# Performance work log

Measured on AMD Instinct MI355X. Metric: run time of the kernel, lower is better.

## Reference

```python
import jax, jax.numpy as jnp
import numpy as np

B, C, H, W = 16, 2, 768, 768
WIN = 5                      # window_size: maxima kernel AND gauss-fit window
PAD = WIN // 2
HEATMAP_AXIS = 1
THRESHOLD = 0.5
MAX_DET = 393216             # fixed-size pad for data-dependent nonzero()


def setup_inputs() -> dict:
    key = jax.random.key(0)
    # strictly positive heat so log(z) in Guo's fit is well-defined
    x = jax.random.uniform(key, (B, C, H, W), dtype=jnp.float32, minval=1e-4, maxval=1.0)
    return {"x": x}


def _forward(x):
    heat = x[:, HEATMAP_AXIS]                                   # [B,H,W]
    th = jnp.where(heat > THRESHOLD, heat, 0.0)
    # kornia dilation with ones kernel (center zeroed) == max over neighbors excl. center
    padded = jnp.pad(th, ((0, 0), (PAD, PAD), (PAD, PAD)), constant_values=-np.inf)
    dilated = jnp.full(th.shape, -np.inf, th.dtype)
    for dy in range(WIN):
        for dx in range(WIN):
            if dy == PAD and dx == PAD:
                continue
            dilated = jnp.maximum(dilated, padded[:, dy:dy + H, dx:dx + W])
    local_max = (th > dilated).reshape(-1)                      # strict local maxima above threshold
    (flat_idx,) = jnp.nonzero(local_max, size=MAX_DET, fill_value=0)  # row-major, like torch.nonzero
    valid = jnp.arange(MAX_DET) < local_max.sum()
    bidx = flat_idx // (H * W)
    rc = flat_idx % (H * W)
    r = rc // W
    cc = rc % W
    sub = jnp.linspace((-WIN) // 2 + 1, WIN // 2, WIN)
    xs, ys = jnp.meshgrid(sub, sub, indexing='xy')              # xs varies along columns
    xf = xs.reshape(-1).astype(jnp.float32)                     # [K]
    yf = ys.reshape(-1).astype(jnp.float32)
    off = jnp.arange(WIN) - PAD
    off_r = jnp.repeat(off, WIN)                                # row-major window flattening
    off_c = jnp.tile(off, WIN)
    rows = jnp.clip(r[:, None] + off_r[None, :], 0, H - 1)      # clamp at borders
    cols = jnp.clip(cc[:, None] + off_c[None, :], 0, W - 1)
    z = heat[bidx[:, None], rows, cols]                         # [N,K] window intensities
    z = jnp.clip(z, 1e-6, None)                                 # numerical guard for log
    xb = jnp.broadcast_to(xf, z.shape)
    yb = jnp.broadcast_to(yf, z.shape)
    # quadratic basis [1, x, x^2, y, xy, y^2]
    basis = jnp.stack([jnp.ones_like(xb), xb, xb * xb, yb, xb * yb, yb * yb], -1)  # [N,K,6]
    wgt = z * z                                                  # Guo's weights
    Aw = basis * wgt[:, :, None]
    bvec = jnp.log(z) * wgt
    ATA = jnp.einsum('nki,nkj->nij', Aw, Aw)                     # [N,6,6]
    ATb = jnp.einsum('nki,nk->ni', Aw, bvec)                     # [N,6]
    coef = jnp.einsum('nij,nj->ni', jnp.linalg.inv(ATA), ATb)    # [N,6]
    Aq, Bl, Cc = coef[:, [2, 5]], coef[:, [1, 3]], coef[:, [0, 4]]
    good = valid & jnp.all(Aq < 0, axis=-1)                      # concave fit -> real sigma
    g = good[:, None]
    Aq_s = jnp.where(g, Aq, -0.5)                                # guard against NaN at padded slots
    sigma = jnp.sqrt(-1.0 / (2.0 * Aq_s))
    mu = Bl * sigma ** 2
    height = jnp.exp(jnp.where(g, Cc + 0.5 * mu ** 2 / sigma ** 2, 0.0))
    pos = jnp.stack([r, cc], -1).astype(jnp.float32) + mu[:, ::-1]  # maxima_indices + mu[:,[1,0]]
    sigma = jnp.where(g, sigma, 0.0)
    pos = jnp.where(g, pos, 0.0)
    height = jnp.where(g, height, 0.0)
    return sigma, pos, height, good


def reference(x):
    return _forward(x)
```

## Files before the change

### kernel.cpp

```cpp
#include <hip/hip_runtime.h>
#include <hip/hip_bf16.h>
#include <cstdint>

#define BATCH 16
#define HDIM 768
#define WDIM 768
#define HW (HDIM * WDIM)
#define NPIX (BATCH * HW)
#define MAX_DET 393216
#define NWORDS (NPIX / 64)
#define SCAT_BLOCKS 576
#define WPB 256

#define MASK_OFF 0u
#define CNT_OFF  1179648u
#define OFF_OFF  1183744u
#define TOT_OFF  1187840u
#define IDX_OFF  1188096u

#define SIGMA_BASE 0
#define POS_BASE   786432
#define HGT_BASE   1572864
#define GOOD_BASE  2359296

#define TILE_C 256
#define TILE_R 32
#define LDS_C 264
#define LDS_R 36
#define VEC_PER_ROW 66
#define TOT_VEC (LDS_R * VEC_PER_ROW)

__device__ __forceinline__ double fast_log_f32(float zf) {
    int ib = __float_as_int(zf);
    int e = ((ib >> 23) & 255) - 127;
    float m1 = __int_as_float((ib & 0x007fffff) | 0x3f800000);
    if (m1 > 1.41421356237f) { m1 *= 0.5f; e += 1; }
    double md = (double)m1;
    double num = md - 1.0;
    double den = md + 1.0;
    double r = (double)__builtin_amdgcn_rcpf((float)den);
    r = r * (2.0 - den * r);
    double s = num * r;
    double t = s * s;
    double P = 1.1111111111111110e-01;
    P = fma(P, t, 1.4285714285714285e-01);
    P = fma(P, t, 2.0000000000000001e-01);
    P = fma(P, t, 3.3333333333333331e-01);
    double s2 = s + s;
    double lm = fma(s2, t * P, s2);
    return fma((double)e, 0.6931471805599453, lm);
}

__device__ __forceinline__ double fast_rcp(double d) {
    double r = (double)__builtin_amdgcn_rcpf((float)d);
    r = r * (2.0 - d * r);
    r = r * (2.0 - d * r);
    return r;
}

__global__ __launch_bounds__(256) void mask_kernel(const float* __restrict__ x,
                                                   unsigned long long* __restrict__ mask) {
    __shared__ float lds[LDS_R * LDS_C];
    const int bid = blockIdx.x;
    const int b   = bid / 72;
    const int rem = bid - b * 72;
    const int rt  = rem / 3;
    const int cs  = rem - rt * 3;
    const int r0  = rt * TILE_R;
    const int tid = threadIdx.x;
    const float* heat = x + (size_t)b * (2 * HW) + HW;

    const int colbase = cs * TILE_C - 4;
    #pragma unroll
    for (int i = 0; i < 10; ++i) {
        int idx = i * 256 + tid;
        if (idx < TOT_VEC) {
            int lr = (unsigned)idx / VEC_PER_ROW;
            int q  = idx - lr * VEC_PER_ROW;
            int row = r0 - 2 + lr;
            int col = colbase + 4 * q;
            float4 v = make_float4(0.f, 0.f, 0.f, 0.f);
            if (row >= 0 && row < HDIM && col >= 0 && col <= WDIM - 4) {
                v = *reinterpret_cast<const float4*>(heat + (size_t)row * WDIM + col);
            }
            float4 t;
            t.x = v.x > 0.5f ? v.x : 0.f;
            t.y = v.y > 0.5f ? v.y : 0.f;
            t.z = v.z > 0.5f ? v.z : 0.f;
            t.w = v.w > 0.5f ? v.w : 0.f;
            *reinterpret_cast<float4*>(&lds[lr * LDS_C + 4 * q]) = t;
        }
    }
    __syncthreads();

    const int wv   = tid >> 6;
    const int lane = tid & 63;
    const int lrow0 = wv * 8;

    auto readrow = [&](int ldsrow, float* h5, float* hx, float* tc) {
        const float* p = &lds[ldsrow * LDS_C + 4 * lane];
        float4 a = *reinterpret_cast<const float4*>(p);
        float4 bb = *reinterpret_cast<const float4*>(p + 4);
        float4 cc = *reinterpret_cast<const float4*>(p + 8);
        float t2=a.z,t3=a.w,t4=bb.x,t5=bb.y,t6=bb.z,t7=bb.w,t8=cc.x,t9=cc.y;
        float pp0=fmaxf(t2,t3), pp1=fmaxf(t3,t4), pp2=fmaxf(t4,t5), pp3=fmaxf(t5,t6),
              pp4=fmaxf(t6,t7), pp5=fmaxf(t7,t8), pp6=fmaxf(t8,t9);
        h5[0]=fmaxf(fmaxf(pp0,pp2),t6);  hx[0]=fmaxf(pp0,pp3);  tc[0]=t4;
        h5[1]=fmaxf(fmaxf(pp1,pp3),t7);  hx[1]=fmaxf(pp1,pp4);  tc[1]=t5;
        h5[2]=fmaxf(fmaxf(pp2,pp4),t8);  hx[2]=fmaxf(pp2,pp5);  tc[2]=t6;
        h5[3]=fmaxf(fmaxf(pp3,pp5),t9);  hx[3]=fmaxf(pp3,pp6);  tc[3]=t7;
    };

    float h5r[5][4], hxr[5][4], tcr[5][4];
    #pragma unroll
    for (int j = 0; j < 4; ++j)
        readrow(lrow0 + j, h5r[j], hxr[j], tcr[j]);

    const int wordbase = b * (HW / 64) + (r0 + wv * 8) * 12 + cs * 4;

    #pragma unroll
    for (int k = 0; k < 8; ++k) {
        readrow(lrow0 + k + 4, h5r[(k+4)%5], hxr[(k+4)%5], tcr[(k+4)%5]);
        unsigned nib = 0;
        #pragma unroll
        for (int c = 0; c < 4; ++c) {
            float dil = fmaxf(fmaxf(h5r[k%5][c], h5r[(k+1)%5][c]),
                        fmaxf(hxr[(k+2)%5][c],
                        fmaxf(h5r[(k+3)%5][c], h5r[(k+4)%5][c])));
            if (tcr[(k+2)%5][c] > dil) nib |= (1u << c);
        }
        unsigned long long w = (unsigned long long)nib << ((lane & 15) * 4);
        w |= __shfl_xor(w, 1);
        w |= __shfl_xor(w, 2);
        w |= __shfl_xor(w, 4);
        w |= __shfl_xor(w, 8);
        if ((lane & 15) == 0) mask[wordbase + k * 12 + (lane >> 4)] = w;
    }
}

__global__ __launch_bounds__(WPB) void count_kernel(const unsigned long long* __restrict__ mask,
                                                    int* __restrict__ counts) {
    __shared__ int s[WPB];
    int t = threadIdx.x;
    int w = blockIdx.x * WPB + t;
    s[t] = __popcll(mask[w]);
    __syncthreads();
    for (int off = WPB / 2; off > 0; off >>= 1) {
        if (t < off) s[t] += s[t + off];
        __syncthreads();
    }
    if (t == 0) counts[blockIdx.x] = s[0];
}

__global__ __launch_bounds__(SCAT_BLOCKS) void scan_kernel(const int* __restrict__ counts,
                                                           int* __restrict__ offsets,
                                                           int* __restrict__ total) {
    __shared__ int s[SCAT_BLOCKS];
    int t = threadIdx.x;
    int my = counts[t];
    s[t] = my;
    __syncthreads();
    for (int off = 1; off < SCAT_BLOCKS; off <<= 1) {
        int add = (t >= off) ? s[t - off] : 0;
        __syncthreads();
        s[t] += add;
        __syncthreads();
    }
    offsets[t] = s[t] - my;
    if (t == SCAT_BLOCKS - 1) *total = s[t];
}

__global__ __launch_bounds__(WPB) void scatter_kernel(const unsigned long long* __restrict__ mask,
                                                      const int* __restrict__ offsets,
                                                      int* __restrict__ flat_idx) {
    __shared__ int s[WPB];
    int t = threadIdx.x;
    int w = blockIdx.x * WPB + t;
    unsigned long long m = mask[w];
    int cnt = __popcll(m);
    s[t] = cnt;
    __syncthreads();
    for (int off = 1; off < WPB; off <<= 1) {
        int add = (t >= off) ? s[t - off] : 0;
        __syncthreads();
        s[t] += add;
        __syncthreads();
    }
    int base = offsets[blockIdx.x] + s[t] - cnt;
    int idx0 = w << 6;
    while (m) {
        int j = __builtin_ctzll(m);
        if (base < MAX_DET) flat_idx[base] = idx0 + j;
        ++base;
        m &= m - 1;
    }
}

__global__ __launch_bounds__(256) void fit_kernel(const float* __restrict__ x,
                                                  const int* __restrict__ flat_idx,
                                                  const int* __restrict__ total,
                                                  float* __restrict__ out) {
    int n = blockIdx.x * 256 + threadIdx.x;
    int count = *total;
    float sx = 0.f, sy = 0.f, p0 = 0.f, p1 = 0.f, h0 = 0.f, h1 = 0.f, goodf = 0.f;
    if (n < count) {
        int idx = flat_idx[n];
        int b = idx / HW;
        int rc = idx - b * HW;
        int r = rc / WDIM;
        int c = rc - r * WDIM;
        const float* heat = x + (size_t)b * (2 * HW) + HW;

        double M00=0,M10=0,M01=0,M20=0,M11=0,M02=0,M30=0,M21=0,M12=0,M03=0;
        double M40=0,M31=0,M22=0,M13=0,M04=0;
        double N0=0,N1=0,N2=0,N3=0,N4=0,N5=0;
        #pragma unroll
        for (int dy = -2; dy <= 2; ++dy) {
            int rr = min(max(r + dy, 0), HDIM - 1);
            const float* hp = heat + (size_t)rr * WDIM;
            double S0=0,S1=0,S2=0,S3=0,S4=0,T0=0,T1=0,T2=0;
            #pragma unroll
            for (int dx = -2; dx <= 2; ++dx) {
                int cc = min(max(c + dx, 0), WDIM - 1);
                float zf = fmaxf(hp[cc], 1e-6f);
                double z = (double)zf;
                double z2 = z * z;
                double w2 = z2 * z2;
                double wl = w2 * fast_log_f32(zf);
                const double X = (double)dx;
                S0 += w2; T0 += wl;
                if (dx != 0) {
                    S1 += w2 * X;
                    S2 += w2 * (X * X);
                    S3 += w2 * (X * X * X);
                    S4 += w2 * (X * X * X * X);
                    T1 += wl * X;
                    T2 += wl * (X * X);
                }
            }
            const double Y = (double)dy;
            M00 += S0; M10 += S1; M20 += S2; M30 += S3; M40 += S4;
            N0 += T0; N1 += T1; N2 += T2;
            if (dy != 0) {
                double Y2 = Y * Y, Y3 = Y2 * Y, Y4 = Y2 * Y2;
                M01 += S0 * Y;  M11 += S1 * Y;  M21 += S2 * Y;  M31 += S3 * Y;
                M02 += S0 * Y2; M12 += S1 * Y2; M22 += S2 * Y2;
                M03 += S0 * Y3; M13 += S1 * Y3;
                M04 += S0 * Y4;
                N3 += T0 * Y; N4 += T1 * Y; N5 += T0 * Y2;
            }
        }

        double A[6][7];
        A[0][0]=M00; A[0][1]=M10; A[0][2]=M20; A[0][3]=M01; A[0][4]=M11; A[0][5]=M02; A[0][6]=N0;
        A[1][0]=M10; A[1][1]=M20; A[1][2]=M30; A[1][3]=M11; A[1][4]=M21; A[1][5]=M12; A[1][6]=N1;
        A[2][0]=M20; A[2][1]=M30; A[2][2]=M40; A[2][3]=M21; A[2][4]=M31; A[2][5]=M22; A[2][6]=N2;
        A[3][0]=M01; A[3][1]=M11; A[3][2]=M21; A[3][3]=M02; A[3][4]=M12; A[3][5]=M03; A[3][6]=N3;
        A[4][0]=M11; A[4][1]=M21; A[4][2]=M31; A[4][3]=M12; A[4][4]=M22; A[4][5]=M13; A[4][6]=N4;
        A[5][0]=M02; A[5][1]=M12; A[5][2]=M22; A[5][3]=M03; A[5][4]=M13; A[5][5]=M04; A[5][6]=N5;

        #pragma unroll
        for (int i = 0; i < 6; ++i) {
            double inv = fast_rcp(A[i][i]);
            #pragma unroll
            for (int j = i + 1; j < 7; ++j) A[i][j] *= inv;
            #pragma unroll
            for (int ii = i + 1; ii < 6; ++ii) {
                double f = A[ii][i];
                #pragma unroll
                for (int j = i + 1; j < 7; ++j) A[ii][j] -= f * A[i][j];
            }
        }
        double cv[6];
        #pragma unroll
        for (int i = 5; i >= 0; --i) {
            double v = A[i][6];
            #pragma unroll
            for (int j = i + 1; j < 6; ++j) v -= A[i][j] * cv[j];
            cv[i] = v;
        }

        double aqx = cv[2], aqy = cv[5];
        if (aqx < 0.0 && aqy < 0.0) {
            double sx2 = -0.5 * fast_rcp(aqx);
            double sy2 = -0.5 * fast_rcp(aqy);
            sx2 = fmin(sx2, 1e300);
            sy2 = fmin(sy2, 1e300);
            double sigx = sqrt(sx2), sigy = sqrt(sy2);
            double mux = cv[1] * sx2, muy = cv[3] * sy2;
            sx = (float)sigx;
            sy = (float)sigy;
            p0 = (float)((double)r + muy);
            p1 = (float)((double)c + mux);
            double hv0 = exp(cv[0] + 0.5 * cv[1] * cv[1] * sx2);
            double hv1 = exp(cv[4] + 0.5 * cv[3] * cv[3] * sy2);
            if (!(hv0 <= 3.0e38)) hv0 = 3.0e38;
            if (!(hv1 <= 3.0e38)) hv1 = 3.0e38;
            h0 = (float)hv0;
            h1 = (float)hv1;
            goodf = 1.0f;
        }
    }
    out[SIGMA_BASE + 2 * n]     = sx;
    out[SIGMA_BASE + 2 * n + 1] = sy;
    out[POS_BASE + 2 * n]       = p0;
    out[POS_BASE + 2 * n + 1]   = p1;
    out[HGT_BASE + 2 * n]       = h0;
    out[HGT_BASE + 2 * n + 1]   = h1;
    out[GOOD_BASE + n]          = goodf;
}

extern "C" void kernel_launch(void* const* d_in, const int* in_sizes, int n_in,
                              void* d_out, int out_size, void* d_ws, size_t ws_size,
                              hipStream_t stream) {
    const float* x = (const float*)d_in[0];
    float* out = (float*)d_out;
    char* ws = (char*)d_ws;

    unsigned long long* mask = (unsigned long long*)(ws + MASK_OFF);
    int* counts  = (int*)(ws + CNT_OFF);
    int* offsets = (int*)(ws + OFF_OFF);
    int* total   = (int*)(ws + TOT_OFF);
    int* flatidx = (int*)(ws + IDX_OFF);

    mask_kernel<<<BATCH * 24 * 3, 256, 0, stream>>>(x, mask);
    count_kernel<<<SCAT_BLOCKS, WPB, 0, stream>>>(mask, counts);
    scan_kernel<<<1, SCAT_BLOCKS, 0, stream>>>(counts, offsets, total);
    scatter_kernel<<<SCAT_BLOCKS, WPB, 0, stream>>>(mask, offsets, flatidx);
    fit_kernel<<<MAX_DET / 256, 256, 0, stream>>>(x, flatidx, total, out);
}
```

Measured before the change: 53.09 us.

## Fold offset scan into scatter kernel and use hardware log/exp2 in fit

Removes the separate single-block scan kernel. Each scatter block now sums the counts of all preceding blocks itself to get its base offset, and block 0 also writes the total. This saves one launch and its serialization, at the cost of redundant prefix reads that grow with block index. The fit kernel also swaps its double-precision log series for the hardware float log, and its double exp for float exp2 with a clamp, which lowers precision.

```diff
diff --git a/kernel.cpp b/kernel.cpp
--- a/kernel.cpp
+++ b/kernel.cpp
@@ -14,7 +14,6 @@
 
 #define MASK_OFF 0u
 #define CNT_OFF  1179648u
-#define OFF_OFF  1183744u
 #define TOT_OFF  1187840u
 #define IDX_OFF  1188096u
 
@@ -34,21 +33,8 @@
     int ib = __float_as_int(zf);
     int e = ((ib >> 23) & 255) - 127;
     float m1 = __int_as_float((ib & 0x007fffff) | 0x3f800000);
-    if (m1 > 1.41421356237f) { m1 *= 0.5f; e += 1; }
-    double md = (double)m1;
-    double num = md - 1.0;
-    double den = md + 1.0;
-    double r = (double)__builtin_amdgcn_rcpf((float)den);
-    r = r * (2.0 - den * r);
-    double s = num * r;
-    double t = s * s;
-    double P = 1.1111111111111110e-01;
-    P = fma(P, t, 1.4285714285714285e-01);
-    P = fma(P, t, 2.0000000000000001e-01);
-    P = fma(P, t, 3.3333333333333331e-01);
-    double s2 = s + s;
-    double lm = fma(s2, t * P, s2);
-    return fma((double)e, 0.6931471805599453, lm);
+    float lg = __builtin_amdgcn_logf(m1);
+    return ((double)e + (double)lg) * 0.6931471805599453;
 }
 
 __device__ __forceinline__ double fast_rcp(double d) {
@@ -152,30 +138,40 @@
     if (t == 0) counts[blockIdx.x] = s[0];
 }
 
-__global__ __launch_bounds__(SCAT_BLOCKS) void scan_kernel(const int* __restrict__ counts,
-                                                           int* __restrict__ offsets,
-                                                           int* __restrict__ total) {
-    __shared__ int s[SCAT_BLOCKS];
-    int t = threadIdx.x;
-    int my = counts[t];
-    s[t] = my;
-    __syncthreads();
-    for (int off = 1; off < SCAT_BLOCKS; off <<= 1) {
-        int add = (t >= off) ? s[t - off] : 0;
-        __syncthreads();
-        s[t] += add;
-        __syncthreads();
-    }
-    offsets[t] = s[t] - my;
-    if (t == SCAT_BLOCKS - 1) *total = s[t];
-}
-
 __global__ __launch_bounds__(WPB) void scatter_kernel(const unsigned long long* __restrict__ mask,
-                                                      const int* __restrict__ offsets,
-                                                      int* __restrict__ flat_idx) {
+                                                      const int* __restrict__ counts,
+                                                      int* __restrict__ flat_idx,
+                                                      int* __restrict__ total) {
     __shared__ int s[WPB];
-    int t = threadIdx.x;
-    int w = blockIdx.x * WPB + t;
+    __shared__ int blockoff;
+    const int t = threadIdx.x;
+    const int bid = blockIdx.x;
+
+    int acc = 0;
+    for (int i = t; i < bid; i += WPB) acc += counts[i];
+    s[t] = acc;
+    __syncthreads();
+    for (int off = WPB / 2; off > 0; off >>= 1) {
+        if (t < off) s[t] += s[t + off];
+        __syncthreads();
+    }
+    if (t == 0) blockoff = s[0];
+    __syncthreads();
+
+    if (bid == 0) {
+        int a2 = 0;
+        for (int i = t; i < SCAT_BLOCKS; i += WPB) a2 += counts[i];
+        s[t] = a2;
+        __syncthreads();
+        for (int off = WPB / 2; off > 0; off >>= 1) {
+            if (t < off) s[t] += s[t + off];
+            __syncthreads();
+        }
+        if (t == 0) *total = s[0];
+        __syncthreads();
+    }
+
+    int w = bid * WPB + t;
     unsigned long long m = mask[w];
     int cnt = __popcll(m);
     s[t] = cnt;
@@ -186,7 +182,7 @@
         s[t] += add;
         __syncthreads();
     }
-    int base = offsets[blockIdx.x] + s[t] - cnt;
+    int base = blockoff + s[t] - cnt;
     int idx0 = w << 6;
     while (m) {
         int j = __builtin_ctzll(m);
@@ -292,12 +288,12 @@
             sy = (float)sigy;
             p0 = (float)((double)r + muy);
             p1 = (float)((double)c + mux);
-            double hv0 = exp(cv[0] + 0.5 * cv[1] * cv[1] * sx2);
-            double hv1 = exp(cv[4] + 0.5 * cv[3] * cv[3] * sy2);
-            if (!(hv0 <= 3.0e38)) hv0 = 3.0e38;
-            if (!(hv1 <= 3.0e38)) hv1 = 3.0e38;
-            h0 = (float)hv0;
-            h1 = (float)hv1;
+            float a0 = (float)((cv[0] + 0.5 * cv[1] * cv[1] * sx2) * 1.4426950408889634);
+            float a1 = (float)((cv[4] + 0.5 * cv[3] * cv[3] * sy2) * 1.4426950408889634);
+            a0 = fminf(a0, 126.0f);
+            a1 = fminf(a1, 126.0f);
+            h0 = exp2f(a0);
+            h1 = exp2f(a1);
             goodf = 1.0f;
         }
     }
@@ -319,13 +315,11 @@
 
     unsigned long long* mask = (unsigned long long*)(ws + MASK_OFF);
     int* counts  = (int*)(ws + CNT_OFF);
-    int* offsets = (int*)(ws + OFF_OFF);
     int* total   = (int*)(ws + TOT_OFF);
     int* flatidx = (int*)(ws + IDX_OFF);
 
     mask_kernel<<<BATCH * 24 * 3, 256, 0, stream>>>(x, mask);
     count_kernel<<<SCAT_BLOCKS, WPB, 0, stream>>>(mask, counts);
-    scan_kernel<<<1, SCAT_BLOCKS, 0, stream>>>(counts, offsets, total);
-    scatter_kernel<<<SCAT_BLOCKS, WPB, 0, stream>>>(mask, offsets, flatidx);
+    scatter_kernel<<<SCAT_BLOCKS, WPB, 0, stream>>>(mask, counts, flatidx, total);
     fit_kernel<<<MAX_DET / 256, 256, 0, stream>>>(x, flatidx, total, out);
 }
```

Result: faster. 48.96 us (-7.8%).
